# Performance work log

Hardware: AMD Instinct MI355X
Metric: run time of the kernel (lower is better)

## Reference

```python
import jax, jax.numpy as jnp
import numpy as np

R_GUIDED = 81      # guided filter radius (kernel 163x163)
EPS = 1e-3
W_COEF = 0.95
MAXV1 = 0.8
BINS = 2000
MINFILT_R = 7      # min-filter radius (kernel 15x15)
NEG_BIG = -1.0e30


def box_mean(x, r):
    # avg_pool2d(kernel=2r+1, stride=1, padding=r, count_include_pad=True)
    # via O(1)-per-pixel integral image. x: [B,H,W]
    k = 2 * r + 1
    xp = jnp.pad(x, ((0, 0), (r, r), (r, r)))
    S = jnp.cumsum(jnp.cumsum(xp, axis=1), axis=2)
    S = jnp.pad(S, ((0, 0), (1, 0), (1, 0)))
    box = S[:, k:, k:] - S[:, :-k, k:] - S[:, k:, :-k] + S[:, :-k, :-k]
    return box / float(k * k)


def min_filter(x, r):
    # -max_pool2d(-x, kernel=2r+1, stride=1, padding=r); torch pads max-pool with -inf
    if r <= 0:
        return x
    k = 2 * r + 1
    return -jax.lax.reduce_window(-x, -jnp.inf, jax.lax.max,
                                  (1, k, k), (1, 1, 1),
                                  [(0, 0), (r, r), (r, r)])


def guided_filter(I, p, r, eps):
    I_mean = box_mean(I, r)
    p_mean = box_mean(p, r)
    Ip_mean = box_mean(I * p, r)
    I_var = box_mean(I * I, r) - I_mean * I_mean
    cov_Ip = Ip_mean - I_mean * p_mean
    a = cov_Ip / (I_var + eps)
    b = p_mean - a * I_mean
    return box_mean(a, r) * I + box_mean(b, r)


def setup_inputs() -> dict:
    key = jax.random.key(0)
    x = jax.random.uniform(key, (8, 3, 768, 1024), dtype=jnp.float32)
    return {"x": x}


def reference(x):
    m = x * 255.0                      # [B,3,H,W]
    V1 = jnp.min(m, axis=1)            # dark channel, [B,H,W]
    V1 = guided_filter(V1, min_filter(V1, MINFILT_R), R_GUIDED, EPS)

    # torch.histc(V1, bins=2000): range [min, max], max value falls in last bin
    mn = jnp.min(V1)
    mx = jnp.max(V1)
    idx = jnp.clip(((V1 - mn) / (mx - mn) * BINS).astype(jnp.int32), 0, BINS - 1)
    hist = jnp.zeros((BINS,), V1.dtype).at[idx.reshape(-1)].add(1.0)
    d = jnp.cumsum(hist) / float(V1.size)
    lmax = jnp.max(jnp.where(d <= 0.999, jnp.arange(BINS), -1))
    thresh = hist[lmax]                # faithful to original: a COUNT used as threshold

    m_mean_c = jnp.mean(m, axis=1)     # [B,H,W]
    mask = V1 >= thresh
    A_cand = jnp.max(jnp.where(mask, m_mean_c, NEG_BIG))
    A_fallback = jnp.max(jnp.mean(m, axis=(1, 2, 3)))
    A = jnp.where(jnp.any(mask), A_cand, A_fallback)

    V1c = jnp.minimum(V1 * W_COEF, MAXV1)           # clamp(max=maxV1)
    Y = (m - V1c[:, None]) / (1.0 - V1c[:, None] / A)
    return jnp.clip(Y, 0.0, 1.0)
```

## Files before the change

kernel.cpp:

```cpp
#include <hip/hip_runtime.h>

#define BATCH 8
#define HH 768
#define WW 1024
#define HW (HH*WW)
#define NPIX (BATCH*HW)
#define RG 81
#define KG (2*RG+1)
#define INVK2 (1.0f/((float)KG*(float)KG))
#define RM 7
#define EPSF 1e-3f
#define NBINS 2000
#define NEG_BIG_F (-1.0e30f)
#define NROWS (BATCH*HH)

#define BH 48
#define NVB 512
#define CHM 32
#define NCHM (HH/CHM)


__device__ inline unsigned fkey(float f) {
    unsigned u = __float_as_uint(f);
    return (u & 0x80000000u) ? ~u : (u | 0x80000000u);
}
__device__ inline float funkey(unsigned k) {
    unsigned u = (k & 0x80000000u) ? (k & 0x7fffffffu) : ~k;
    return __uint_as_float(u);
}

__device__ inline void bandDecode(int idx, int& img, int& c, int& h0) {
    img = idx & 7;
    int j = idx >> 3;
    int colq = j >> 4;
    int band = j & 15;
    c = colq * 256 + threadIdx.x;
    h0 = band * BH;
}

__device__ inline float waveInclScan(float x) {
    int lane = threadIdx.x & 63;
#pragma unroll
    for (int d = 1; d < 64; d <<= 1) {
        float u = __shfl_up(x, (unsigned)d, 64);
        if (lane >= d) x += u;
    }
    return x;
}

__device__ inline void scanRow(float v0, float v1, float v2, float v3,
                               float* cum, float* wsum) {
    int tid = threadIdx.x;
    float c0 = v0, c1 = c0 + v1, c2 = c1 + v2, c3 = c2 + v3;
    float inc = waveInclScan(c3);
    int lane = tid & 63, wv = tid >> 6;
    if (lane == 63) wsum[wv] = inc;
    __syncthreads();
    float basev = 0.f;
    if (wv > 0) basev += wsum[0];
    if (wv > 1) basev += wsum[1];
    if (wv > 2) basev += wsum[2];
    float ex = basev + inc - c3;
    cum[4 * tid + 0] = ex + c0;
    cum[4 * tid + 1] = ex + c1;
    cum[4 * tid + 2] = ex + c2;
    cum[4 * tid + 3] = ex + c3;
}


__global__ __launch_bounds__(256) void k_prep(const float* __restrict__ x,
                                              float* __restrict__ V1raw,
                                              float* __restrict__ mmean,
                                              float* __restrict__ hmin,
                                              float* __restrict__ pbsum,
                                              unsigned* __restrict__ scal,
                                              unsigned* __restrict__ hist) {
    int t = threadIdx.x;
    if (blockIdx.x == 0) {
        for (int i = t; i < NBINS; i += 256) hist[i] = 0u;
        if (t == 0) {
            scal[0] = 0xFFFFFFFFu;
            scal[1] = 0u;
            scal[2] = 0u;
            scal[3] = 0u;
        }
    }
    int img = blockIdx.x / HH;
    int row = blockIdx.x % HH;
    int pix = row * WW + t * 4;
    size_t base = (size_t)img * 3 * HW + pix;
    float4 c0 = *(const float4*)(x + base);
    float4 c1 = *(const float4*)(x + base + HW);
    float4 c2 = *(const float4*)(x + base + 2 * (size_t)HW);
    float4 mnv, mev;
    {
        float a0 = c0.x * 255.0f, a1 = c1.x * 255.0f, a2 = c2.x * 255.0f;
        mnv.x = fminf(a0, fminf(a1, a2)); mev.x = (a0 + a1 + a2) * (1.0f / 3.0f);
        a0 = c0.y * 255.0f; a1 = c1.y * 255.0f; a2 = c2.y * 255.0f;
        mnv.y = fminf(a0, fminf(a1, a2)); mev.y = (a0 + a1 + a2) * (1.0f / 3.0f);
        a0 = c0.z * 255.0f; a1 = c1.z * 255.0f; a2 = c2.z * 255.0f;
        mnv.z = fminf(a0, fminf(a1, a2)); mev.z = (a0 + a1 + a2) * (1.0f / 3.0f);
        a0 = c0.w * 255.0f; a1 = c1.w * 255.0f; a2 = c2.w * 255.0f;
        mnv.w = fminf(a0, fminf(a1, a2)); mev.w = (a0 + a1 + a2) * (1.0f / 3.0f);
    }
    size_t po = (size_t)img * HW + pix;
    *(float4*)(V1raw + po) = mnv;
    *(float4*)(mmean + po) = mev;

    __shared__ float r[WW];
    r[4 * t + 0] = mnv.x; r[4 * t + 1] = mnv.y; r[4 * t + 2] = mnv.z; r[4 * t + 3] = mnv.w;

    float s = mev.x + mev.y + mev.z + mev.w;
#pragma unroll
    for (int d = 32; d >= 1; d >>= 1) s += __shfl_down(s, (unsigned)d, 64);
    __shared__ float wsum[4];
    int lane = t & 63, wv = t >> 6;
    if (lane == 0) wsum[wv] = s;
    __syncthreads();
    if (t == 0)
        pbsum[blockIdx.x] = wsum[0] + wsum[1] + wsum[2] + wsum[3];

    float v[18];
#pragma unroll
    for (int i = 0; i < 18; i++) {
        int w = 4 * t - RM + i;
        w = w < 0 ? 0 : (w > WW - 1 ? WW - 1 : w);
        v[i] = r[w];
    }
#pragma unroll
    for (int i = 0; i < 17; i++) v[i] = fminf(v[i], v[i + 1]);
#pragma unroll
    for (int i = 0; i < 15; i++) v[i] = fminf(v[i], v[i + 2]);
#pragma unroll
    for (int i = 0; i < 11; i++) v[i] = fminf(v[i], v[i + 4]);
    float4 o;
    o.x = fminf(v[0], v[7]);
    o.y = fminf(v[1], v[8]);
    o.z = fminf(v[2], v[9]);
    o.w = fminf(v[3], v[10]);
    *(float4*)(hmin + po) = o;
}

__global__ __launch_bounds__(256) void k_minv(const float* __restrict__ in,
                                              float* __restrict__ out) {
    int g = blockIdx.x * 256 + threadIdx.x;
    int w = g & (WW - 1);
    int t = g >> 10;
    int b = t / NCHM;
    int ch = t - b * NCHM;
    int h0 = ch * CHM;
    const float* col = in + (size_t)b * HW + w;
    float* ocol = out + (size_t)b * HW + w;
    float v[CHM + 14];
#pragma unroll
    for (int i = 0; i < CHM + 14; i++) {
        int h = h0 - RM + i;
        h = h < 0 ? 0 : (h > HH - 1 ? HH - 1 : h);
        v[i] = col[(size_t)h * WW];
    }
#pragma unroll
    for (int i = 0; i < CHM + 13; i++) v[i] = fminf(v[i], v[i + 1]);
#pragma unroll
    for (int i = 0; i < CHM + 11; i++) v[i] = fminf(v[i], v[i + 2]);
#pragma unroll
    for (int i = 0; i < CHM + 7; i++)  v[i] = fminf(v[i], v[i + 4]);
#pragma unroll
    for (int i = 0; i < CHM; i++)
        ocol[(size_t)(h0 + i) * WW] = fminf(v[i], v[i + 7]);
}

__global__ __launch_bounds__(256) void k_kv1(const float* __restrict__ I,
                                             const float* __restrict__ p,
                                             float4* __restrict__ F4) {
    int img, c, h0;
    bandDecode(blockIdx.x, img, c, h0);
    const float* bI = I + (size_t)img * HW + c;
    const float* bP = p + (size_t)img * HW + c;
    float4* bO = F4 + (size_t)img * HW + c;

    float4 A = {0,0,0,0};
    int jlo = h0 - RG; if (jlo < 0) jlo = 0;
    int jhi = h0 + RG - 1; if (jhi > HH - 1) jhi = HH - 1;
    {
        float Li[8], Lp[8];
        int j = jlo;
        for (; j + 7 <= jhi; j += 8) {
#pragma unroll
            for (int k = 0; k < 8; k++) {
                Li[k] = bI[(size_t)(j + k) * WW];
                Lp[k] = bP[(size_t)(j + k) * WW];
            }
#pragma unroll
            for (int k = 0; k < 8; k++) {
                A.x += Li[k]; A.y += Lp[k]; A.z += Li[k] * Lp[k]; A.w += Li[k] * Li[k];
            }
        }
        for (; j <= jhi; j++) {
            float a = bI[(size_t)j * WW], q = bP[(size_t)j * WW];
            A.x += a; A.y += q; A.z += a * q; A.w += a * a;
        }
    }

    float Ai[8], Ap[8], Si[8], Sp[8];
    for (int h = h0; h < h0 + BH; h += 8) {
#pragma unroll
        for (int k = 0; k < 8; k++) {
            int ra = h + k + RG;
            int ca = ra <= HH - 1 ? ra : HH - 1;
            float a = bI[(size_t)ca * WW];
            float q = bP[(size_t)ca * WW];
            if (ra > HH - 1) { a = 0.f; q = 0.f; }
            Ai[k] = a; Ap[k] = q;
        }
#pragma unroll
        for (int k = 0; k < 8; k++) {
            int rs = h + k - RG;
            int cs = rs >= 0 ? rs : 0;
            float a = bI[(size_t)cs * WW];
            float q = bP[(size_t)cs * WW];
            if (rs < 0) { a = 0.f; q = 0.f; }
            Si[k] = a; Sp[k] = q;
        }
#pragma unroll
        for (int k = 0; k < 8; k++) {
            A.x += Ai[k]; A.y += Ap[k]; A.z += Ai[k] * Ap[k]; A.w += Ai[k] * Ai[k];
            bO[(size_t)(h + k) * WW] = A;
            A.x -= Si[k]; A.y -= Sp[k]; A.z -= Si[k] * Sp[k]; A.w -= Si[k] * Si[k];
        }
    }
}

__global__ __launch_bounds__(256) void k_kh1(const float4* __restrict__ F4,
                                             float2* __restrict__ HAB) {
    __shared__ float cI[WW], cP[WW], cIp[WW], cII[WW];
    __shared__ float cA[WW], cB[WW];
    __shared__ float w0[4], w1[4], w2[4], w3[4], w4[4], w5[4];
    size_t base = (size_t)blockIdx.x * WW;
    int t = threadIdx.x;
    float4 q0 = F4[base + 4 * t + 0];
    float4 q1 = F4[base + 4 * t + 1];
    float4 q2 = F4[base + 4 * t + 2];
    float4 q3 = F4[base + 4 * t + 3];
    scanRow(q0.x, q1.x, q2.x, q3.x, cI, w0);
    scanRow(q0.y, q1.y, q2.y, q3.y, cP, w1);
    scanRow(q0.z, q1.z, q2.z, q3.z, cIp, w2);
    scanRow(q0.w, q1.w, q2.w, q3.w, cII, w3);
    __syncthreads();
    float av[4], bv[4];
#pragma unroll
    for (int j = 0; j < 4; j++) {
        int w = 4 * t + j;
        int hi = w + RG; if (hi > WW - 1) hi = WW - 1;
        int lo = w - RG - 1;
        float a = cI[hi], b = cP[hi], c = cIp[hi], d = cII[hi];
        if (lo >= 0) { a -= cI[lo]; b -= cP[lo]; c -= cIp[lo]; d -= cII[lo]; }
        float mI = a * INVK2, mP = b * INVK2, mIp = c * INVK2, mII = d * INVK2;
        float aa = (mIp - mI * mP) / ((mII - mI * mI) + EPSF);
        av[j] = aa; bv[j] = mP - aa * mI;
    }
    __syncthreads();
    scanRow(av[0], av[1], av[2], av[3], cA, w4);
    scanRow(bv[0], bv[1], bv[2], bv[3], cB, w5);
    __syncthreads();
    float oa[4], ob[4];
#pragma unroll
    for (int j = 0; j < 4; j++) {
        int w = 4 * t + j;
        int hi = w + RG; if (hi > WW - 1) hi = WW - 1;
        int lo = w - RG - 1;
        float a = cA[hi], b = cB[hi];
        if (lo >= 0) { a -= cA[lo]; b -= cB[lo]; }
        oa[j] = a; ob[j] = b;
    }
    ((float4*)(HAB + base))[2 * t]     = make_float4(oa[0], ob[0], oa[1], ob[1]);
    ((float4*)(HAB + base))[2 * t + 1] = make_float4(oa[2], ob[2], oa[3], ob[3]);
}

__global__ __launch_bounds__(256) void k_kv2(const float2* __restrict__ HAB,
                                             const float* __restrict__ I,
                                             float* __restrict__ V1,
                                             unsigned* __restrict__ scal) {
    int img, c, h0;
    bandDecode(blockIdx.x, img, c, h0);
    const float2* bC = HAB + (size_t)img * HW + c;
    const float* bI = I + (size_t)img * HW + c;
    float* bV = V1 + (size_t)img * HW + c;

    float2 s0 = {0,0}, s1 = {0,0}, s2 = {0,0}, s3 = {0,0};
    int jlo = h0 - RG; if (jlo < 0) jlo = 0;
    int jhi = h0 + RG - 1; if (jhi > HH - 1) jhi = HH - 1;
    {
        float2 L[8];
        int j = jlo;
        for (; j + 7 <= jhi; j += 8) {
#pragma unroll
            for (int k = 0; k < 8; k++) L[k] = bC[(size_t)(j + k) * WW];
            s0.x += L[0].x; s0.y += L[0].y;
            s1.x += L[1].x; s1.y += L[1].y;
            s2.x += L[2].x; s2.y += L[2].y;
            s3.x += L[3].x; s3.y += L[3].y;
            s0.x += L[4].x; s0.y += L[4].y;
            s1.x += L[5].x; s1.y += L[5].y;
            s2.x += L[6].x; s2.y += L[6].y;
            s3.x += L[7].x; s3.y += L[7].y;
        }
        for (; j <= jhi; j++) {
            float2 v = bC[(size_t)j * WW];
            s0.x += v.x; s0.y += v.y;
        }
    }
    float2 acc;
    acc.x = (s0.x + s1.x) + (s2.x + s3.x);
    acc.y = (s0.y + s1.y) + (s2.y + s3.y);

    float lmn = 3.4e38f, lmx = -3.4e38f;
    float2 A[8], S[8];
    float Iv[8];
    for (int h = h0; h < h0 + BH; h += 8) {
#pragma unroll
        for (int k = 0; k < 8; k++) {
            int ra = h + k + RG;
            int ca = ra <= HH - 1 ? ra : HH - 1;
            float2 v = bC[(size_t)ca * WW];
            if (ra > HH - 1) v = make_float2(0.f, 0.f);
            A[k] = v;
        }
#pragma unroll
        for (int k = 0; k < 8; k++) {
            int rs = h + k - RG;
            int cs = rs >= 0 ? rs : 0;
            float2 v = bC[(size_t)cs * WW];
            if (rs < 0) v = make_float2(0.f, 0.f);
            S[k] = v;
        }
#pragma unroll
        for (int k = 0; k < 8; k++) Iv[k] = bI[(size_t)(h + k) * WW];
#pragma unroll
        for (int k = 0; k < 8; k++) {
            acc.x += A[k].x; acc.y += A[k].y;
            float v0 = acc.x * INVK2 * Iv[k] + acc.y * INVK2;
            bV[(size_t)(h + k) * WW] = v0;
            lmn = fminf(lmn, v0);
            lmx = fmaxf(lmx, v0);
            acc.x -= S[k].x; acc.y -= S[k].y;
        }
    }
#pragma unroll
    for (int d = 32; d >= 1; d >>= 1) {
        lmn = fminf(lmn, __shfl_down(lmn, (unsigned)d, 64));
        lmx = fmaxf(lmx, __shfl_down(lmx, (unsigned)d, 64));
    }
    __shared__ float smn[4], smx[4];
    int lane = threadIdx.x & 63, wv = threadIdx.x >> 6;
    if (lane == 0) { smn[wv] = lmn; smx[wv] = lmx; }
    __syncthreads();
    if (threadIdx.x == 0) {
        float a = fminf(fminf(smn[0], smn[1]), fminf(smn[2], smn[3]));
        float b = fmaxf(fmaxf(smx[0], smx[1]), fmaxf(smx[2], smx[3]));
        atomicMin(&scal[0], fkey(a));
        atomicMax(&scal[1], fkey(b));
    }
}

__global__ __launch_bounds__(256) void k_hist(const float* __restrict__ V1,
                                              const unsigned* __restrict__ scal,
                                              unsigned* __restrict__ hist) {
    __shared__ unsigned lh[NBINS];
    for (int i = threadIdx.x; i < NBINS; i += 256) lh[i] = 0u;
    __syncthreads();
    float mn = funkey(scal[0]);
    float mx = funkey(scal[1]);
    float inv = 2000.0f / (mx - mn);
    const float4* V4 = (const float4*)V1;
    for (int i = blockIdx.x * 256 + threadIdx.x; i < NPIX / 4; i += gridDim.x * 256) {
        float4 v = V4[i];
        int i0 = (int)((v.x - mn) * inv); i0 = i0 < 0 ? 0 : (i0 > NBINS - 1 ? NBINS - 1 : i0);
        int i1 = (int)((v.y - mn) * inv); i1 = i1 < 0 ? 0 : (i1 > NBINS - 1 ? NBINS - 1 : i1);
        int i2 = (int)((v.z - mn) * inv); i2 = i2 < 0 ? 0 : (i2 > NBINS - 1 ? NBINS - 1 : i2);
        int i3 = (int)((v.w - mn) * inv); i3 = i3 < 0 ? 0 : (i3 > NBINS - 1 ? NBINS - 1 : i3);
        atomicAdd(&lh[i0], 1u);
        atomicAdd(&lh[i1], 1u);
        atomicAdd(&lh[i2], 1u);
        atomicAdd(&lh[i3], 1u);
    }
    __syncthreads();
    for (int i = threadIdx.x; i < NBINS; i += 256) {
        unsigned c = lh[i];
        if (c) atomicAdd(&hist[i], c);
    }
}

__global__ __launch_bounds__(256) void k_amax(const float* __restrict__ V1,
                                              const float* __restrict__ mmean,
                                              const unsigned* __restrict__ hist,
                                              unsigned* __restrict__ scal) {
    __shared__ float wsum[4];
    __shared__ int smaxi[4];
    __shared__ float sthresh;
    int t = threadIdx.x;
    int lane = t & 63, wv = t >> 6;
    {
        unsigned h[8];
        float local = 0.f;
#pragma unroll
        for (int j = 0; j < 8; j++) {
            int idx = t * 8 + j;
            h[j] = (idx < NBINS) ? hist[idx] : 0u;
            local += (float)h[j];
        }
        float inc = waveInclScan(local);
        if (lane == 63) wsum[wv] = inc;
        __syncthreads();
        float basev = 0.f;
        if (wv > 0) basev += wsum[0];
        if (wv > 1) basev += wsum[1];
        if (wv > 2) basev += wsum[2];
        float cum = basev + inc - local;
        int lmax = -1;
#pragma unroll
        for (int j = 0; j < 8; j++) {
            int idx = t * 8 + j;
            cum += (float)h[j];
            float d = cum / (float)NPIX;
            if (idx < NBINS && d <= 0.999f) lmax = idx;
        }
#pragma unroll
        for (int d = 32; d >= 1; d >>= 1) {
            int o = __shfl_down(lmax, (unsigned)d, 64);
            lmax = o > lmax ? o : lmax;
        }
        if (lane == 0) smaxi[wv] = lmax;
        __syncthreads();
        if (t == 0) {
            int m = smaxi[0];
            if (smaxi[1] > m) m = smaxi[1];
            if (smaxi[2] > m) m = smaxi[2];
            if (smaxi[3] > m) m = smaxi[3];
            int idx = m < 0 ? NBINS - 1 : m;
            sthresh = (float)hist[idx];
        }
        __syncthreads();
    }
    float th = sthresh;

    float lmax = NEG_BIG_F;
    bool any = false;
    const float4* V4 = (const float4*)V1;
    const float4* M4 = (const float4*)mmean;
    for (int i = blockIdx.x * 256 + t; i < NPIX / 4; i += gridDim.x * 256) {
        float4 v = V4[i];
        if (v.x >= th || v.y >= th || v.z >= th || v.w >= th) {
            float4 m = M4[i];
            any = true;
            if (v.x >= th) lmax = fmaxf(lmax, m.x);
            if (v.y >= th) lmax = fmaxf(lmax, m.y);
            if (v.z >= th) lmax = fmaxf(lmax, m.z);
            if (v.w >= th) lmax = fmaxf(lmax, m.w);
        }
    }
#pragma unroll
    for (int d = 32; d >= 1; d >>= 1) lmax = fmaxf(lmax, __shfl_down(lmax, (unsigned)d, 64));
    unsigned long long ab = __ballot(any);
    __shared__ float smx[4];
    __shared__ unsigned sany[4];
    if (lane == 0) { smx[wv] = lmax; sany[wv] = ab ? 1u : 0u; }
    __syncthreads();
    if (t == 0) {
        float m = fmaxf(fmaxf(smx[0], smx[1]), fmaxf(smx[2], smx[3]));
        unsigned a = sany[0] | sany[1] | sany[2] | sany[3];
        if (a) {
            atomicOr(&scal[3], 1u);
            atomicMax(&scal[2], fkey(m));
        }
    }
}

__global__ __launch_bounds__(256) void k_selA(const unsigned* __restrict__ scal,
                                              const float* __restrict__ pbsum,
                                              float* __restrict__ fscal) {
    __shared__ double simg[BATCH];
    __shared__ double ws[4];
    int t = threadIdx.x;
    int lane = t & 63, wv = t >> 6;
    for (int img = 0; img < BATCH; img++) {
        const float* p = pbsum + img * HH;
        double s = (double)p[t] + (double)p[t + 256] + (double)p[t + 512];
#pragma unroll
        for (int d = 32; d >= 1; d >>= 1) s += __shfl_down(s, (unsigned)d, 64);
        if (lane == 0) ws[wv] = s;
        __syncthreads();
        if (t == 0) simg[img] = ws[0] + ws[1] + ws[2] + ws[3];
        __syncthreads();
    }
    if (t == 0) {
        float A;
        if (scal[3]) {
            A = funkey(scal[2]);
        } else {
            double best = -1e300;
            for (int b = 0; b < BATCH; b++) {
                double m = simg[b] / (double)HW;
                if (m > best) best = m;
            }
            A = (float)best;
        }
        fscal[5] = A;
    }
}

__global__ __launch_bounds__(256) void k_final(const float* __restrict__ x,
                                               const float* __restrict__ V1,
                                               const float* __restrict__ fscal,
                                               float* __restrict__ out) {
    float A = fscal[5];
    float invA = 1.0f / A;
    int i = (blockIdx.x * 256 + threadIdx.x) * 4;
    int b = i / HW;
    int pix = i - b * HW;
    float4 v1 = *(const float4*)(V1 + i);
    float4 v1c, den;
    v1c.x = fminf(v1.x * 0.95f, 0.8f); den.x = 1.0f / (1.0f - v1c.x * invA);
    v1c.y = fminf(v1.y * 0.95f, 0.8f); den.y = 1.0f / (1.0f - v1c.y * invA);
    v1c.z = fminf(v1.z * 0.95f, 0.8f); den.z = 1.0f / (1.0f - v1c.z * invA);
    v1c.w = fminf(v1.w * 0.95f, 0.8f); den.w = 1.0f / (1.0f - v1c.w * invA);
    size_t o = (size_t)b * 3 * HW + pix;
#pragma unroll
    for (int c = 0; c < 3; c++) {
        float4 m = *(const float4*)(x + o);
        float4 y;
        y.x = fminf(fmaxf((m.x * 255.0f - v1c.x) * den.x, 0.0f), 1.0f);
        y.y = fminf(fmaxf((m.y * 255.0f - v1c.y) * den.y, 0.0f), 1.0f);
        y.z = fminf(fmaxf((m.z * 255.0f - v1c.z) * den.z, 0.0f), 1.0f);
        y.w = fminf(fmaxf((m.w * 255.0f - v1c.w) * den.w, 0.0f), 1.0f);
        *(float4*)(out + o) = y;
        o += HW;
    }
}


extern "C" void kernel_launch(void* const* d_in, const int* in_sizes, int n_in,
                              void* d_out, int out_size, void* d_ws, size_t ws_size,
                              hipStream_t stream) {
    const float* x = (const float*)d_in[0];
    float* out = (float*)d_out;

    unsigned* scal = (unsigned*)d_ws;
    float* fscal = (float*)d_ws;
    unsigned* hist = (unsigned*)((char*)d_ws + 96);
    float* pbsum = (float*)((char*)d_ws + 8192);
    float* planes = (float*)((char*)d_ws + 131072);
    float* P0 = planes + (size_t)0 * NPIX;
    float* P1 = planes + (size_t)1 * NPIX;
    float* P2 = planes + (size_t)2 * NPIX;
    float* P3 = planes + (size_t)3 * NPIX;
    float* P6 = planes + (size_t)6 * NPIX;
    float4* F4 = (float4*)(planes + (size_t)4 * NPIX);
    float2* HAB = (float2*)P2;

    k_prep<<<NROWS, 256, 0, stream>>>(x, P0, P1, P2, pbsum, scal, hist);
    k_minv<<<BATCH * NCHM * WW / 256, 256, 0, stream>>>(P2, P3);
    k_kv1<<<NVB, 256, 0, stream>>>(P0, P3, F4);
    k_kh1<<<NROWS, 256, 0, stream>>>(F4, HAB);
    k_kv2<<<NVB, 256, 0, stream>>>(HAB, P0, P6, scal);
    k_hist<<<1024, 256, 0, stream>>>(P6, scal, hist);
    k_amax<<<1024, 256, 0, stream>>>(P6, P1, hist, scal);
    k_selA<<<1, 256, 0, stream>>>(scal, pbsum, fscal);
    k_final<<<NPIX / 1024, 256, 0, stream>>>(x, P6, fscal, out);
}
```

Measured before the change: 237.0 us.

## Fuse vertical and horizontal guided-filter box passes into one kernel

```diff
diff --git a/kernel.cpp b/kernel.cpp
--- a/kernel.cpp
+++ b/kernel.cpp
@@ -16,6 +16,8 @@
 
 #define BH 48
 #define NVB 512
+#define BH1 24
+#define NVB1 (BATCH*(HH/BH1))
 #define CHM 32
 #define NCHM (HH/CHM)
 
@@ -65,6 +67,26 @@
     cum[4 * tid + 1] = ex + c1;
     cum[4 * tid + 2] = ex + c2;
     cum[4 * tid + 3] = ex + c3;
+}
+
+__device__ inline void scanRow512(float v0, float v1, float* cum, float* wsum) {
+    int tid = threadIdx.x;
+    float c0 = v0, c1 = c0 + v1;
+    float inc = waveInclScan(c1);
+    int lane = tid & 63, wv = tid >> 6;
+    if (lane == 63) wsum[wv] = inc;
+    __syncthreads();
+    float basev = 0.f;
+    if (wv > 0) basev += wsum[0];
+    if (wv > 1) basev += wsum[1];
+    if (wv > 2) basev += wsum[2];
+    if (wv > 3) basev += wsum[3];
+    if (wv > 4) basev += wsum[4];
+    if (wv > 5) basev += wsum[5];
+    if (wv > 6) basev += wsum[6];
+    float ex = basev + inc - c1;
+    cum[2 * tid]     = ex + c0;
+    cum[2 * tid + 1] = ex + c1;
 }
 
 
@@ -169,111 +191,114 @@
         ocol[(size_t)(h0 + i) * WW] = fminf(v[i], v[i + 7]);
 }
 
-__global__ __launch_bounds__(256) void k_kv1(const float* __restrict__ I,
-                                             const float* __restrict__ p,
-                                             float4* __restrict__ F4) {
-    int img, c, h0;
-    bandDecode(blockIdx.x, img, c, h0);
+__global__ __launch_bounds__(512) void k_kvh1(const float* __restrict__ I,
+                                              const float* __restrict__ p,
+                                              float2* __restrict__ HAB) {
+    __shared__ float cI[WW], cP[WW], cIp[WW], cII[WW], cA[WW], cB[WW];
+    __shared__ float w0[8], w1[8], w2[8], w3[8], w4[8], w5[8];
+    int img = blockIdx.x & 7;
+    int band = blockIdx.x >> 3;
+    int h0 = band * BH1;
+    int t = threadIdx.x;
+    int c = 2 * t;
     const float* bI = I + (size_t)img * HW + c;
     const float* bP = p + (size_t)img * HW + c;
-    float4* bO = F4 + (size_t)img * HW + c;
-
-    float4 A = {0,0,0,0};
+    float* bO = (float*)(HAB + (size_t)img * HW);
+
+    float4 A = {0,0,0,0}, B = {0,0,0,0};
     int jlo = h0 - RG; if (jlo < 0) jlo = 0;
     int jhi = h0 + RG - 1; if (jhi > HH - 1) jhi = HH - 1;
     {
-        float Li[8], Lp[8];
+        float2 Li[8], Lp[8];
         int j = jlo;
         for (; j + 7 <= jhi; j += 8) {
 #pragma unroll
             for (int k = 0; k < 8; k++) {
-                Li[k] = bI[(size_t)(j + k) * WW];
-                Lp[k] = bP[(size_t)(j + k) * WW];
+                Li[k] = *(const float2*)(bI + (size_t)(j + k) * WW);
+                Lp[k] = *(const float2*)(bP + (size_t)(j + k) * WW);
             }
 #pragma unroll
             for (int k = 0; k < 8; k++) {
-                A.x += Li[k]; A.y += Lp[k]; A.z += Li[k] * Lp[k]; A.w += Li[k] * Li[k];
+                A.x += Li[k].x; A.y += Lp[k].x; A.z += Li[k].x * Lp[k].x; A.w += Li[k].x * Li[k].x;
+                B.x += Li[k].y; B.y += Lp[k].y; B.z += Li[k].y * Lp[k].y; B.w += Li[k].y * Li[k].y;
             }
         }
         for (; j <= jhi; j++) {
-            float a = bI[(size_t)j * WW], q = bP[(size_t)j * WW];
-            A.x += a; A.y += q; A.z += a * q; A.w += a * a;
-        }
-    }
-
-    float Ai[8], Ap[8], Si[8], Sp[8];
-    for (int h = h0; h < h0 + BH; h += 8) {
-#pragma unroll
-        for (int k = 0; k < 8; k++) {
-            int ra = h + k + RG;
-            int ca = ra <= HH - 1 ? ra : HH - 1;
-            float a = bI[(size_t)ca * WW];
-            float q = bP[(size_t)ca * WW];
-            if (ra > HH - 1) { a = 0.f; q = 0.f; }
-            Ai[k] = a; Ap[k] = q;
-        }
-#pragma unroll
-        for (int k = 0; k < 8; k++) {
-            int rs = h + k - RG;
-            int cs = rs >= 0 ? rs : 0;
-            float a = bI[(size_t)cs * WW];
-            float q = bP[(size_t)cs * WW];
-            if (rs < 0) { a = 0.f; q = 0.f; }
-            Si[k] = a; Sp[k] = q;
-        }
-#pragma unroll
-        for (int k = 0; k < 8; k++) {
-            A.x += Ai[k]; A.y += Ap[k]; A.z += Ai[k] * Ap[k]; A.w += Ai[k] * Ai[k];
-            bO[(size_t)(h + k) * WW] = A;
-            A.x -= Si[k]; A.y -= Sp[k]; A.z -= Si[k] * Sp[k]; A.w -= Si[k] * Si[k];
-        }
-    }
-}
-
-__global__ __launch_bounds__(256) void k_kh1(const float4* __restrict__ F4,
-                                             float2* __restrict__ HAB) {
-    __shared__ float cI[WW], cP[WW], cIp[WW], cII[WW];
-    __shared__ float cA[WW], cB[WW];
-    __shared__ float w0[4], w1[4], w2[4], w3[4], w4[4], w5[4];
-    size_t base = (size_t)blockIdx.x * WW;
-    int t = threadIdx.x;
-    float4 q0 = F4[base + 4 * t + 0];
-    float4 q1 = F4[base + 4 * t + 1];
-    float4 q2 = F4[base + 4 * t + 2];
-    float4 q3 = F4[base + 4 * t + 3];
-    scanRow(q0.x, q1.x, q2.x, q3.x, cI, w0);
-    scanRow(q0.y, q1.y, q2.y, q3.y, cP, w1);
-    scanRow(q0.z, q1.z, q2.z, q3.z, cIp, w2);
-    scanRow(q0.w, q1.w, q2.w, q3.w, cII, w3);
-    __syncthreads();
-    float av[4], bv[4];
-#pragma unroll
-    for (int j = 0; j < 4; j++) {
-        int w = 4 * t + j;
-        int hi = w + RG; if (hi > WW - 1) hi = WW - 1;
-        int lo = w - RG - 1;
-        float a = cI[hi], b = cP[hi], c = cIp[hi], d = cII[hi];
-        if (lo >= 0) { a -= cI[lo]; b -= cP[lo]; c -= cIp[lo]; d -= cII[lo]; }
-        float mI = a * INVK2, mP = b * INVK2, mIp = c * INVK2, mII = d * INVK2;
-        float aa = (mIp - mI * mP) / ((mII - mI * mI) + EPSF);
-        av[j] = aa; bv[j] = mP - aa * mI;
-    }
-    __syncthreads();
-    scanRow(av[0], av[1], av[2], av[3], cA, w4);
-    scanRow(bv[0], bv[1], bv[2], bv[3], cB, w5);
-    __syncthreads();
-    float oa[4], ob[4];
-#pragma unroll
-    for (int j = 0; j < 4; j++) {
-        int w = 4 * t + j;
-        int hi = w + RG; if (hi > WW - 1) hi = WW - 1;
-        int lo = w - RG - 1;
-        float a = cA[hi], b = cB[hi];
-        if (lo >= 0) { a -= cA[lo]; b -= cB[lo]; }
-        oa[j] = a; ob[j] = b;
-    }
-    ((float4*)(HAB + base))[2 * t]     = make_float4(oa[0], ob[0], oa[1], ob[1]);
-    ((float4*)(HAB + base))[2 * t + 1] = make_float4(oa[2], ob[2], oa[3], ob[3]);
+            float2 a = *(const float2*)(bI + (size_t)j * WW);
+            float2 q = *(const float2*)(bP + (size_t)j * WW);
+            A.x += a.x; A.y += q.x; A.z += a.x * q.x; A.w += a.x * a.x;
+            B.x += a.y; B.y += q.y; B.z += a.y * q.y; B.w += a.y * a.y;
+        }
+    }
+
+    float2 ai, ap, si, sp;
+    {
+        int ra = h0 + RG; int ca = ra <= HH - 1 ? ra : HH - 1;
+        ai = *(const float2*)(bI + (size_t)ca * WW);
+        ap = *(const float2*)(bP + (size_t)ca * WW);
+        if (ra > HH - 1) { ai = make_float2(0.f, 0.f); ap = make_float2(0.f, 0.f); }
+        int rs = h0 - RG; int cs = rs >= 0 ? rs : 0;
+        si = *(const float2*)(bI + (size_t)cs * WW);
+        sp = *(const float2*)(bP + (size_t)cs * WW);
+        if (rs < 0) { si = make_float2(0.f, 0.f); sp = make_float2(0.f, 0.f); }
+    }
+    for (int h = h0; h < h0 + BH1; h++) {
+        float2 nai = make_float2(0.f, 0.f), nap = nai, nsi = nai, nsp = nai;
+        if (h + 1 < h0 + BH1) {
+            int ra = h + 1 + RG; int ca = ra <= HH - 1 ? ra : HH - 1;
+            nai = *(const float2*)(bI + (size_t)ca * WW);
+            nap = *(const float2*)(bP + (size_t)ca * WW);
+            if (ra > HH - 1) { nai = make_float2(0.f, 0.f); nap = make_float2(0.f, 0.f); }
+            int rs = h + 1 - RG; int cs = rs >= 0 ? rs : 0;
+            nsi = *(const float2*)(bI + (size_t)cs * WW);
+            nsp = *(const float2*)(bP + (size_t)cs * WW);
+            if (rs < 0) { nsi = make_float2(0.f, 0.f); nsp = make_float2(0.f, 0.f); }
+        }
+        A.x += ai.x; A.y += ap.x; A.z += ai.x * ap.x; A.w += ai.x * ai.x;
+        B.x += ai.y; B.y += ap.y; B.z += ai.y * ap.y; B.w += ai.y * ai.y;
+
+        scanRow512(A.x, B.x, cI, w0);
+        scanRow512(A.y, B.y, cP, w1);
+        scanRow512(A.z, B.z, cIp, w2);
+        scanRow512(A.w, B.w, cII, w3);
+        __syncthreads();
+        float av0, bv0, av1, bv1;
+        {
+            int hi = c + RG; if (hi > WW - 1) hi = WW - 1;
+            int lo = c - RG - 1;
+            float a = cI[hi], b = cP[hi], d = cIp[hi], e = cII[hi];
+            if (lo >= 0) { a -= cI[lo]; b -= cP[lo]; d -= cIp[lo]; e -= cII[lo]; }
+            float mI = a * INVK2, mP = b * INVK2, mIp = d * INVK2, mII = e * INVK2;
+            av0 = (mIp - mI * mP) / ((mII - mI * mI) + EPSF);
+            bv0 = mP - av0 * mI;
+            int w = c + 1;
+            hi = w + RG; if (hi > WW - 1) hi = WW - 1;
+            lo = w - RG - 1;
+            a = cI[hi]; b = cP[hi]; d = cIp[hi]; e = cII[hi];
+            if (lo >= 0) { a -= cI[lo]; b -= cP[lo]; d -= cIp[lo]; e -= cII[lo]; }
+            mI = a * INVK2; mP = b * INVK2; mIp = d * INVK2; mII = e * INVK2;
+            av1 = (mIp - mI * mP) / ((mII - mI * mI) + EPSF);
+            bv1 = mP - av1 * mI;
+        }
+        scanRow512(av0, av1, cA, w4);
+        scanRow512(bv0, bv1, cB, w5);
+        __syncthreads();
+        {
+            int hi = c + RG; if (hi > WW - 1) hi = WW - 1;
+            int lo = c - RG - 1;
+            float ha0 = cA[hi], hb0 = cB[hi];
+            if (lo >= 0) { ha0 -= cA[lo]; hb0 -= cB[lo]; }
+            int w = c + 1;
+            hi = w + RG; if (hi > WW - 1) hi = WW - 1;
+            lo = w - RG - 1;
+            float ha1 = cA[hi], hb1 = cB[hi];
+            if (lo >= 0) { ha1 -= cA[lo]; hb1 -= cB[lo]; }
+            *(float4*)(bO + 2 * ((size_t)h * WW) + 2 * c) = make_float4(ha0, hb0, ha1, hb1);
+        }
+        A.x -= si.x; A.y -= sp.x; A.z -= si.x * sp.x; A.w -= si.x * si.x;
+        B.x -= si.y; B.y -= sp.y; B.z -= si.y * sp.y; B.w -= si.y * si.y;
+        ai = nai; ap = nap; si = nsi; sp = nsp;
+    }
 }
 
 __global__ __launch_bounds__(256) void k_kv2(const float2* __restrict__ HAB,
@@ -554,13 +579,11 @@
     float* P2 = planes + (size_t)2 * NPIX;
     float* P3 = planes + (size_t)3 * NPIX;
     float* P6 = planes + (size_t)6 * NPIX;
-    float4* F4 = (float4*)(planes + (size_t)4 * NPIX);
-    float2* HAB = (float2*)P2;
+    float2* HAB = (float2*)(planes + (size_t)4 * NPIX);
 
     k_prep<<<NROWS, 256, 0, stream>>>(x, P0, P1, P2, pbsum, scal, hist);
     k_minv<<<BATCH * NCHM * WW / 256, 256, 0, stream>>>(P2, P3);
-    k_kv1<<<NVB, 256, 0, stream>>>(P0, P3, F4);
-    k_kh1<<<NROWS, 256, 0, stream>>>(F4, HAB);
+    k_kvh1<<<NVB1, 512, 0, stream>>>(P0, P3, HAB);
     k_kv2<<<NVB, 256, 0, stream>>>(HAB, P0, P6, scal);
     k_hist<<<1024, 256, 0, stream>>>(P6, scal, hist);
     k_amax<<<1024, 256, 0, stream>>>(P6, P1, hist, scal);
```

Result: slower. 257.9 us (+8.8%).
